# Kernel tuning notes

Hardware: AMD Instinct MI355X
Metric: run time of the kernel (lower is better)

The kernel has to match this reference:

```python
import jax, jax.numpy as jnp
import numpy as np

N_USERS = 100000
N_ITEMS = 50000
N_NODES = N_USERS + N_ITEMS
N_EDGES = 4800000
EMB_DIM = 64
N_LAYERS = 3


def setup_inputs() -> dict:
    key = jax.random.key(0)
    k1, k2, k3, k4, k5 = jax.random.split(key, 5)
    user_emb = jax.random.normal(k1, (N_USERS, EMB_DIM), dtype=jnp.float32)
    item_emb = jax.random.normal(k2, (N_ITEMS, EMB_DIM), dtype=jnp.float32)
    # COO representation of the (symmetric-normalized) adjacency matrix
    edge_src = jax.random.randint(k3, (N_EDGES,), 0, N_NODES, dtype=jnp.int32)
    edge_dst = jax.random.randint(k4, (N_EDGES,), 0, N_NODES, dtype=jnp.int32)
    edge_weight = jax.random.uniform(k5, (N_EDGES,), dtype=jnp.float32)
    return {
        "user_emb": user_emb,
        "item_emb": item_emb,
        "edge_weight": edge_weight,
        "edge_src": edge_src,
        "edge_dst": edge_dst,
    }


def _spmm(edge_src, edge_dst, edge_weight, x):
    # out[i] = sum_j A[i, j] * x[j]  with A in COO (dst=row i, src=col j)
    msgs = edge_weight[:, None] * x[edge_src]  # [E, D]
    return jax.ops.segment_sum(msgs, edge_dst, num_segments=N_NODES)


def reference(user_emb, item_emb, edge_weight, edge_src, edge_dst):
    ego = jnp.concatenate([user_emb, item_emb], axis=0)  # [N, D]
    acc = ego  # running sum over layer embeddings (layer 0 included)
    for _ in range(N_LAYERS):
        ego = _spmm(edge_src, edge_dst, edge_weight, ego)
        acc = acc + ego
    mean_emb = acc / jnp.float32(N_LAYERS + 1)  # mean over (L+1) layers
    new_user = mean_emb[:N_USERS]
    new_item = mean_emb[N_USERS:]
    return new_user, new_item
```

## Files before the change

### kernel.cpp

```cpp
#include <hip/hip_runtime.h>
#include <hip/hip_fp16.h>

#define N_USERS 100000
#define N_ITEMS 50000
#define N_NODES 150000
#define N_EDGES 4800000
#define EMB 64
#define N_LAYERS 3

#define NBKT 512
#define NPB  293
#define NREP 8
#define SUBCAP 1536
#define CAP (NREP * SUBCAP)
#define P1GRID 2344
#define INITGRID 9375

typedef unsigned int u32;
typedef unsigned short u16;
typedef u32 vu4 __attribute__((ext_vector_type(4)));
typedef u32 vu2 __attribute__((ext_vector_type(2)));
typedef float vf4 __attribute__((ext_vector_type(4)));

#define W_BITS 14
#define W_SCALE 16384.0f
#define W_INV   (1.0f / 16384.0f)
#define W_MASK  16383u

__device__ __forceinline__ float hh(u16 v) {
    return __half2float(__ushort_as_half(v));
}

struct Dec4 { u32 r0, r1, r2, r3; float w0, w1, w2, w3; };

__device__ __forceinline__ Dec4 dec_fast(vu4 p) {
    Dec4 d;
    d.r0 = p.x >> W_BITS; d.w0 = (float)(p.x & W_MASK);
    d.r1 = p.y >> W_BITS; d.w1 = (float)(p.y & W_MASK);
    d.r2 = p.z >> W_BITS; d.w2 = (float)(p.z & W_MASK);
    d.r3 = p.w >> W_BITS; d.w3 = (float)(p.w & W_MASK);
    return d;
}

__device__ __forceinline__ Dec4 dec_mask(vu4 p, int eb, int beg, int end) {
    Dec4 d;
    bool v0 = (eb + 0 >= beg) && (eb + 0 < end);
    bool v1 = (eb + 1 >= beg) && (eb + 1 < end);
    bool v2 = (eb + 2 >= beg) && (eb + 2 < end);
    bool v3 = (eb + 3 >= beg) && (eb + 3 < end);
    d.r0 = v0 ? (p.x >> W_BITS) : 0u; d.w0 = v0 ? (float)(p.x & W_MASK) : 0.f;
    d.r1 = v1 ? (p.y >> W_BITS) : 0u; d.w1 = v1 ? (float)(p.y & W_MASK) : 0.f;
    d.r2 = v2 ? (p.z >> W_BITS) : 0u; d.w2 = v2 ? (float)(p.z & W_MASK) : 0.f;
    d.r3 = v3 ? (p.w >> W_BITS) : 0u; d.w3 = v3 ? (float)(p.w & W_MASK) : 0.f;
    return d;
}

__device__ __forceinline__ Dec4 dec(vu4 p, int lo, int beg, int end, int g) {
    if (lo >= beg && lo + 16 <= end) return dec_fast(p);
    return dec_mask(p, lo + 4 * g, beg, end);
}

__device__ __forceinline__ vu4 ldp(const u32* p) {
    return __builtin_nontemporal_load((const vu4*)p);
}

__device__ __forceinline__ vu2 ldx(const char* xbase, u32 r, u32 moff) {
    return *(const vu2*)(xbase + (size_t)(r * 128u + moff));
}

__device__ __forceinline__ void fmix2(float& a0, float& a1, float w, u32 x) {
    asm("v_fma_mix_f32 %0, %1, %2, %0 op_sel:[0,0,0] op_sel_hi:[0,1,0]"
        : "+v"(a0) : "v"(w), "v"(x));
    asm("v_fma_mix_f32 %0, %1, %2, %0 op_sel:[0,1,0] op_sel_hi:[0,1,0]"
        : "+v"(a1) : "v"(w), "v"(x));
}

__device__ __forceinline__ void acc4(vu2 xv, float w,
                                     float& ax, float& ay, float& az, float& aw) {
    fmix2(ax, ay, w, xv.x);
    fmix2(az, aw, w, xv.y);
}

#define LOADX(pfx, d) \
    vu2 pfx##0 = ldx(xbase, d.r0, moff), pfx##1 = ldx(xbase, d.r1, moff), \
        pfx##2 = ldx(xbase, d.r2, moff), pfx##3 = ldx(xbase, d.r3, moff)
#define ACCX(pfx, d) \
    acc4(pfx##0, d.w0, ax, ay, az, aw); acc4(pfx##1, d.w1, ax, ay, az, aw); \
    acc4(pfx##2, d.w2, ax, ay, az, aw); acc4(pfx##3, d.w3, ax, ay, az, aw)
#define RED(v) v += __shfl_xor(v, 16); v += __shfl_xor(v, 32)

__global__ __launch_bounds__(256) void k_build1(const int4*   __restrict__ src4,
                                                const int4*   __restrict__ dst4,
                                                const float4* __restrict__ w4,
                                                int* __restrict__ cursor,
                                                u32* __restrict__ pk_arr,
                                                u16* __restrict__ ld_arr,
                                                const float4* __restrict__ user,
                                                const float4* __restrict__ item,
                                                ushort4* __restrict__ h0) {
    int tid = threadIdx.x;

    if (blockIdx.x >= P1GRID) {
        int i = (int)(blockIdx.x - P1GRID) * 256 + tid;
        const int total4 = N_NODES * EMB / 4;
        const int user4  = N_USERS * EMB / 4;
        if (i >= total4) return;
        float4 v = (i < user4) ? user[i] : item[i - user4];
        ushort4 h;
        h.x = __half_as_ushort(__float2half_rn(v.x));
        h.y = __half_as_ushort(__float2half_rn(v.y));
        h.z = __half_as_ushort(__float2half_rn(v.z));
        h.w = __half_as_ushort(__float2half_rn(v.w));
        h0[i] = h;
        return;
    }

    __shared__ int hist[NBKT];
    __shared__ int base[NBKT];
    __shared__ int bscan[NBKT];
    __shared__ int wsum[256];
    __shared__ u32 s_pk[2048];
    __shared__ u32 s_meta[2048];
    hist[tid] = 0;
    hist[tid + 256] = 0;
    __syncthreads();

    int g0 = blockIdx.x * 512 + tid * 2;
    bool act = (g0 < N_EDGES / 4);

    u32 pk[8];
    u32 meta[8];
    int rk[8];
    if (act) {
        int4 d0 = dst4[g0], d1 = dst4[g0 + 1];
        int4 s0 = src4[g0], s1 = src4[g0 + 1];
        float4 f0 = w4[g0], f1 = w4[g0 + 1];
        int   ds[8] = {d0.x, d0.y, d0.z, d0.w, d1.x, d1.y, d1.z, d1.w};
        int   ss[8] = {s0.x, s0.y, s0.z, s0.w, s1.x, s1.y, s1.z, s1.w};
        float wf[8] = {f0.x, f0.y, f0.z, f0.w, f1.x, f1.y, f1.z, f1.w};
        #pragma unroll
        for (int k = 0; k < 8; ++k) {
            u32 d  = (u32)ds[k];
            u32 b  = d / NPB;
            u32 ld = d - b * NPB;
            rk[k]  = atomicAdd(&hist[b], 1);
            u32 wq = (u32)(wf[k] * W_SCALE + 0.5f);
            if (wq > W_MASK) wq = W_MASK;
            pk[k]   = ((u32)ss[k] << W_BITS) | wq;
            meta[k] = (b << 10) | ld;
        }
    }
    __syncthreads();

    int rep = blockIdx.x & (NREP - 1);
    int hA = hist[tid];
    int hB = hist[tid + 256];
    if (hA > 0) base[tid]       = atomicAdd(&cursor[rep * NBKT + tid], hA);
    if (hB > 0) base[tid + 256] = atomicAdd(&cursor[rep * NBKT + tid + 256], hB);

    int a0 = hist[2 * tid];
    int a1 = hist[2 * tid + 1];
    wsum[tid] = a0 + a1;
    __syncthreads();
    for (int off = 1; off < 256; off <<= 1) {
        int t = 0;
        if (tid >= off) t = wsum[tid - off];
        __syncthreads();
        if (tid >= off) wsum[tid] += t;
        __syncthreads();
    }
    int exclp = wsum[tid] - (a0 + a1);
    bscan[2 * tid]     = exclp + a0;
    bscan[2 * tid + 1] = exclp + a0 + a1;
    __syncthreads();

    if (act) {
        #pragma unroll
        for (int k = 0; k < 8; ++k) {
            u32 b = meta[k] >> 10;
            int s = (bscan[b] - hist[b]) + rk[k];
            s_pk[s]   = pk[k];
            s_meta[s] = meta[k];
        }
    }
    __syncthreads();

    int total = bscan[NBKT - 1];
    #pragma unroll
    for (int k = 0; k < 8; ++k) {
        int s = k * 256 + tid;
        if (s < total) {
            u32 mt = s_meta[s];
            u32 b  = mt >> 10;
            int pos = base[b] + (s - (bscan[b] - hist[b]));
            if (pos < SUBCAP) {
                size_t slot = (size_t)b * CAP + (size_t)rep * SUBCAP + pos;
                pk_arr[slot] = s_pk[s];
                ld_arr[slot] = (u16)(mt & 1023u);
            }
        }
    }
}

extern __shared__ u32 s_pk2[];

__global__ __launch_bounds__(1024) void k_p2g(const int* __restrict__ cursor,
                                              const u32* __restrict__ pk_arr,
                                              const u16* __restrict__ ld_arr,
                                              int* __restrict__ row_ptr,
                                              u32* __restrict__ pairs,
                                              const __half* __restrict__ x,
                                              __half* __restrict__ nxt) {
    __shared__ int hist[1024];
    __shared__ int start[NPB];
    __shared__ int rbeg[NPB];
    __shared__ int rend[NPB];
    __shared__ int btot[NBKT];
    __shared__ int bsum[NBKT];
    int b = blockIdx.x;
    int tid = threadIdx.x;
    hist[tid] = 0;
    if (tid < NBKT) {
        int s = 0;
        #pragma unroll
        for (int r = 0; r < NREP; ++r) s += cursor[r * NBKT + tid];
        btot[tid] = s;
        bsum[tid] = s;
    }
    if (b == 0 && tid == 0) row_ptr[N_NODES] = N_EDGES;
    __syncthreads();
    for (int off = 1; off < NBKT; off <<= 1) {
        int t = 0;
        if (tid < NBKT && tid >= off) t = bsum[tid - off];
        __syncthreads();
        if (tid < NBKT && tid >= off) bsum[tid] += t;
        __syncthreads();
    }
    int gbase = bsum[b] - btot[b];

    int lo = b * NPB;
    int nbn = N_NODES - lo; if (nbn > NPB) nbn = NPB;

    int n[NREP];
    #pragma unroll
    for (int r = 0; r < NREP; ++r) {
        int c = cursor[r * NBKT + b];
        n[r] = (c > SUBCAP) ? SUBCAP : c;
    }

    for (int r = 0; r < NREP; ++r) {
        const u16* p = ld_arr + (size_t)b * CAP + (size_t)r * SUBCAP;
        for (int i = tid; i < n[r]; i += 1024)
            atomicAdd(&hist[p[i]], 1);
    }
    __syncthreads();

    int val = hist[tid];
    for (int off = 1; off < 1024; off <<= 1) {
        int t = 0;
        if (tid >= off) t = hist[tid - off];
        __syncthreads();
        if (tid >= off) hist[tid] += t;
        __syncthreads();
    }
    int excl = hist[tid] - val;
    if (tid < nbn) row_ptr[lo + tid] = gbase + excl;
    if (tid < NPB) {
        start[tid] = excl;
        rbeg[tid]  = excl;
        rend[tid]  = hist[tid];
    }
    __syncthreads();

    for (int r = 0; r < NREP; ++r) {
        const u16* p = ld_arr + (size_t)b * CAP + (size_t)r * SUBCAP;
        const u32* q = pk_arr + (size_t)b * CAP + (size_t)r * SUBCAP;
        for (int i = tid; i < n[r]; i += 1024) {
            int slot = atomicAdd(&start[p[i]], 1);
            s_pk2[slot] = q[i];
        }
    }
    __syncthreads();

    int total = hist[1023];
    if (tid < 16) s_pk2[total + tid] = 0;
    for (int s = tid; s < total; s += 1024)
        pairs[gbase + s] = s_pk2[s];
    __syncthreads();

    int wid  = tid >> 6;
    int lane = tid & 63;
    const int m = lane & 15;
    const int g = lane >> 4;
    const u32 moff = (u32)m << 3;
    const char* xbase = (const char*)x;

    for (int row = wid; row < nbn; row += 16) {
        int beg = rbeg[row];
        int end = rend[row];
        float ax = 0.f, ay = 0.f, az = 0.f, aw = 0.f;
        int jb = beg & ~3;
        int nb = (end - jb + 15) >> 4;
        const u32* pp = s_pk2 + jb + 4 * g;

        if (nb == 1) {
            vu4 P0 = *(const vu4*)pp;
            Dec4 d0 = dec(P0, jb, beg, end, g);
            LOADX(xa, d0);
            ACCX(xa, d0);
        } else if (nb == 2) {
            vu4 P0 = *(const vu4*)pp;
            vu4 P1 = *(const vu4*)(pp + 16);
            Dec4 d0 = dec(P0, jb, beg, end, g);
            LOADX(xa, d0);
            Dec4 d1 = dec(P1, jb + 16, beg, end, g);
            LOADX(xc, d1);
            ACCX(xa, d0);
            ACCX(xc, d1);
        } else if (nb == 3) {
            vu4 P0 = *(const vu4*)pp;
            vu4 P1 = *(const vu4*)(pp + 16);
            vu4 P2 = *(const vu4*)(pp + 32);
            Dec4 d0 = dec(P0, jb, beg, end, g);
            LOADX(xa, d0);
            Dec4 d1 = dec(P1, jb + 16, beg, end, g);
            LOADX(xc, d1);
            ACCX(xa, d0);
            Dec4 d2 = dec(P2, jb + 32, beg, end, g);
            LOADX(xd, d2);
            ACCX(xc, d1);
            ACCX(xd, d2);
        } else if (nb >= 4) {
            vu4 P0 = *(const vu4*)pp;
            vu4 P1 = *(const vu4*)(pp + 16);
            vu4 P2 = *(const vu4*)(pp + 32);
            Dec4 d0 = dec(P0, jb, beg, end, g);
            LOADX(xa, d0);
            Dec4 d1 = dec(P1, jb + 16, beg, end, g);
            LOADX(xc, d1);
            ACCX(xa, d0);
            vu4 P3 = *(const vu4*)(pp + 48);
            Dec4 d2 = dec(P2, jb + 32, beg, end, g);
            LOADX(xd, d2);
            ACCX(xc, d1);
            Dec4 d3 = dec(P3, jb + 48, beg, end, g);
            LOADX(xe, d3);
            ACCX(xd, d2);
            ACCX(xe, d3);
            for (int t = 4; t < nb; ++t) {
                vu4 Pl = *(const vu4*)(pp + (size_t)16 * t);
                Dec4 dl = dec(Pl, jb + 16 * t, beg, end, g);
                LOADX(xf, dl);
                ACCX(xf, dl);
            }
        }

        RED(ax); RED(ay); RED(az); RED(aw);

        if (lane < 16) {
            ushort4 h;
            h.x = __half_as_ushort(__float2half_rn(ax * W_INV));
            h.y = __half_as_ushort(__float2half_rn(ay * W_INV));
            h.z = __half_as_ushort(__float2half_rn(az * W_INV));
            h.w = __half_as_ushort(__float2half_rn(aw * W_INV));
            ((ushort4*)nxt)[(size_t)(lo + row) * 16 + m] = h;
        }
    }
}

template<int FIN>
__global__ __launch_bounds__(256) void k_gather(const int* __restrict__ row_ptr,
                                                const u32* __restrict__ pairs,
                                                const __half* __restrict__ x,
                                                __half* __restrict__ nxt,
                                                const ushort4* __restrict__ e0,
                                                const ushort4* __restrict__ e1,
                                                const ushort4* __restrict__ e2,
                                                float* __restrict__ outp) {
    int wave = (blockIdx.x * blockDim.x + threadIdx.x) >> 6;
    int lane = threadIdx.x & 63;
    if (wave >= N_NODES) return;

    const int m = lane & 15;
    ushort4 ega = {}, ea = {}, eb = {};
    if (FIN && lane < 16) {
        size_t idx = (size_t)wave * 16 + m;
        ega = e0[idx]; ea = e1[idx]; eb = e2[idx];
    }

    int beg = row_ptr[wave];
    int end = row_ptr[wave + 1];

    const int g = lane >> 4;
    const u32 moff = (u32)m << 3;
    const char* xbase = (const char*)x;

    float ax = 0.f, ay = 0.f, az = 0.f, aw = 0.f;

    int jb = beg & ~3;
    int nb = (end - jb + 15) >> 4;
    const u32* pp = pairs + jb + 4 * g;

    if (nb == 1) {
        vu4 P0 = ldp(pp);
        Dec4 d0 = dec(P0, jb, beg, end, g);
        LOADX(xa, d0);
        ACCX(xa, d0);
    } else if (nb == 2) {
        vu4 P0 = ldp(pp);
        vu4 P1 = ldp(pp + 16);
        Dec4 d0 = dec(P0, jb, beg, end, g);
        LOADX(xa, d0);
        Dec4 d1 = dec(P1, jb + 16, beg, end, g);
        LOADX(xc, d1);
        ACCX(xa, d0);
        ACCX(xc, d1);
    } else if (nb == 3) {
        vu4 P0 = ldp(pp);
        vu4 P1 = ldp(pp + 16);
        vu4 P2 = ldp(pp + 32);
        Dec4 d0 = dec(P0, jb, beg, end, g);
        LOADX(xa, d0);
        Dec4 d1 = dec(P1, jb + 16, beg, end, g);
        LOADX(xc, d1);
        ACCX(xa, d0);
        Dec4 d2 = dec(P2, jb + 32, beg, end, g);
        LOADX(xd, d2);
        ACCX(xc, d1);
        ACCX(xd, d2);
    } else if (nb >= 4) {
        vu4 P0 = ldp(pp);
        vu4 P1 = ldp(pp + 16);
        vu4 P2 = ldp(pp + 32);
        Dec4 d0 = dec(P0, jb, beg, end, g);
        LOADX(xa, d0);
        Dec4 d1 = dec(P1, jb + 16, beg, end, g);
        LOADX(xc, d1);
        ACCX(xa, d0);
        vu4 P3 = ldp(pp + 48);
        Dec4 d2 = dec(P2, jb + 32, beg, end, g);
        LOADX(xd, d2);
        ACCX(xc, d1);
        Dec4 d3 = dec(P3, jb + 48, beg, end, g);
        LOADX(xe, d3);
        ACCX(xd, d2);
        ACCX(xe, d3);
        for (int t = 4; t < nb; ++t) {
            vu4 Pl = ldp(pp + (size_t)16 * t);
            Dec4 dl = dec(Pl, jb + 16 * t, beg, end, g);
            LOADX(xf, dl);
            ACCX(xf, dl);
        }
    }

    RED(ax); RED(ay); RED(az); RED(aw);

    if (lane < 16) {
        if (FIN) {
            vf4 o;
            o.x = (hh(ega.x) + hh(ea.x) + hh(eb.x) + ax * W_INV) * 0.25f;
            o.y = (hh(ega.y) + hh(ea.y) + hh(eb.y) + ay * W_INV) * 0.25f;
            o.z = (hh(ega.z) + hh(ea.z) + hh(eb.z) + az * W_INV) * 0.25f;
            o.w = (hh(ega.w) + hh(ea.w) + hh(eb.w) + aw * W_INV) * 0.25f;
            __builtin_nontemporal_store(o, (vf4*)outp + (size_t)wave * 16 + m);
        } else {
            ushort4 h;
            h.x = __half_as_ushort(__float2half_rn(ax * W_INV));
            h.y = __half_as_ushort(__float2half_rn(ay * W_INV));
            h.z = __half_as_ushort(__float2half_rn(az * W_INV));
            h.w = __half_as_ushort(__float2half_rn(aw * W_INV));
            ((ushort4*)nxt)[(size_t)wave * 16 + m] = h;
        }
    }
}

__global__ void k_spmm(const int*   __restrict__ src,
                       const int*   __restrict__ dst,
                       const float* __restrict__ w,
                       const float* __restrict__ x,
                       float*       __restrict__ y) {
    long long t = (long long)blockIdx.x * blockDim.x + threadIdx.x;
    int e = (int)(t >> 4);
    if (e >= N_EDGES) return;
    int q = (int)(t & 15);
    int   s  = src[e];
    int   d  = dst[e];
    float we = w[e];
    const float4* xs = (const float4*)(x + (long long)s * EMB);
    float4 v = xs[q];
    float* yd = y + (long long)d * EMB + q * 4;
    atomicAdd(yd + 0, we * v.x);
    atomicAdd(yd + 1, we * v.y);
    atomicAdd(yd + 2, we * v.z);
    atomicAdd(yd + 3, we * v.w);
}

__global__ void k_init_f32(const float4* __restrict__ user,
                           const float4* __restrict__ item,
                           float4* __restrict__ out,
                           float4* __restrict__ cur) {
    int i = blockIdx.x * blockDim.x + threadIdx.x;
    const int total4 = N_NODES * EMB / 4;
    const int user4  = N_USERS * EMB / 4;
    if (i >= total4) return;
    float4 v = (i < user4) ? user[i] : item[i - user4];
    out[i] = v;
    cur[i] = v;
}

__global__ void k_acc(float4* __restrict__ out,
                      const float4* __restrict__ buf,
                      float scale) {
    int i = blockIdx.x * blockDim.x + threadIdx.x;
    const int total4 = N_NODES * EMB / 4;
    if (i >= total4) return;
    float4 o = out[i];
    float4 b = buf[i];
    o.x = (o.x + b.x) * scale;
    o.y = (o.y + b.y) * scale;
    o.z = (o.z + b.z) * scale;
    o.w = (o.w + b.w) * scale;
    out[i] = o;
}

extern "C" void kernel_launch(void* const* d_in, const int* in_sizes, int n_in,
                              void* d_out, int out_size, void* d_ws, size_t ws_size,
                              hipStream_t stream) {
    const float* user_emb = (const float*)d_in[0];
    const float* item_emb = (const float*)d_in[1];
    const float* edge_w   = (const float*)d_in[2];
    const int*   edge_src = (const int*)d_in[3];
    const int*   edge_dst = (const int*)d_in[4];
    float* out = (float*)d_out;

    const size_t feat_elems = (size_t)N_NODES * EMB;
    const size_t feat_bytes_f32 = feat_elems * 4;
    const size_t feat_bytes_f16 = feat_elems * 2;

    char* ws = (char*)d_ws;
    size_t off = 0;
    __half* h0 = (__half*)(ws + off); off += feat_bytes_f16;
    __half* h1 = (__half*)(ws + off); off += feat_bytes_f16;
    __half* h2 = (__half*)(ws + off); off += feat_bytes_f16;
    int* row_ptr  = (int*)(ws + off); off += ((size_t)(N_NODES + 1) * 4 + 63) / 64 * 64;
    int* cursor   = (int*)(ws + off); off += (size_t)NREP * NBKT * 4;
    u32* pk_arr = (u32*)(ws + off);   off += (size_t)NBKT * CAP * 4;
    u16* ld_arr = (u16*)(ws + off);   off += (size_t)NBKT * CAP * 2;
    u32* pairs  = (u32*)(ws + off);   off += (size_t)N_EDGES * 4 + 64;
    const size_t needed = off;

    const int block = 256;
    const int total4 = (int)(feat_elems / 4);
    const int fgrid = (total4 + block - 1) / block;
    const int bgrid = P1GRID + INITGRID;
    const int ggrid = (N_NODES + 3) / 4;

    if (ws_size >= needed) {
        (void)hipMemsetAsync(cursor, 0, (size_t)NREP * NBKT * 4, stream);

        k_build1<<<bgrid, block, 0, stream>>>((const int4*)edge_src,
                                              (const int4*)edge_dst,
                                              (const float4*)edge_w,
                                              cursor, pk_arr, ld_arr,
                                              (const float4*)user_emb,
                                              (const float4*)item_emb,
                                              (ushort4*)h0);
        k_p2g<<<NBKT, 1024, (size_t)(CAP + 16) * 4, stream>>>(cursor, pk_arr,
                                                              ld_arr, row_ptr,
                                                              pairs, h0, h1);

        k_gather<0><<<ggrid, block, 0, stream>>>(row_ptr, pairs, h1, h2,
                                                 nullptr, nullptr, nullptr,
                                                 nullptr);
        k_gather<1><<<ggrid, block, 0, stream>>>(row_ptr, pairs, h2, nullptr,
                                                 (const ushort4*)h0,
                                                 (const ushort4*)h1,
                                                 (const ushort4*)h2,
                                                 out);
    } else {
        float* buf0 = (float*)d_ws;
        float* buf1 = buf0 + feat_elems;
        k_init_f32<<<fgrid, block, 0, stream>>>((const float4*)user_emb,
                                                (const float4*)item_emb,
                                                (float4*)out, (float4*)buf0);
        float* cur = buf0;
        float* nxt = buf1;
        for (int layer = 0; layer < N_LAYERS; ++layer) {
            (void)hipMemsetAsync(nxt, 0, feat_bytes_f32, stream);
            long long threads = (long long)N_EDGES * 16;
            int grid = (int)((threads + block - 1) / block);
            k_spmm<<<grid, block, 0, stream>>>(edge_src, edge_dst, edge_w, cur, nxt);
            float scale = (layer == N_LAYERS - 1) ? (1.0f / (N_LAYERS + 1)) : 1.0f;
            k_acc<<<fgrid, block, 0, stream>>>((float4*)out, (const float4*)nxt, scale);
            float* tmp = cur; cur = nxt; nxt = tmp;
        }
    }
}
```

Baseline: 416.4 us.

## Fuse CSR build and all three gather layers into one cooperative kernel

Adds a cooperative kernel in which each of the 512 blocks builds its bucket's CSR edge list in shared memory, then runs all three propagation layers from that shared-memory copy, using grid-wide syncs between layers. This drops writing and re-reading the global row_ptr/pairs arrays and two extra kernel launches. The final layer fuses the layer mean into the output write. The cost is that occupancy is fixed at 512 resident blocks of 1024 threads, plus grid-barrier overhead. If the cooperative launch fails, it falls back to the old three-kernel path.

Result: slower. 1.001 ms (+140.5%).

```diff
diff --git a/kernel.cpp b/kernel.cpp
--- a/kernel.cpp
+++ b/kernel.cpp
@@ -1,5 +1,8 @@
 #include <hip/hip_runtime.h>
 #include <hip/hip_fp16.h>
+#include <hip/hip_cooperative_groups.h>
+
+namespace cg = cooperative_groups;
 
 #define N_USERS 100000
 #define N_ITEMS 50000
@@ -89,205 +92,18 @@
     acc4(pfx##2, d.w2, ax, ay, az, aw); acc4(pfx##3, d.w3, ax, ay, az, aw)
 #define RED(v) v += __shfl_xor(v, 16); v += __shfl_xor(v, 32)
 
-__global__ __launch_bounds__(256) void k_build1(const int4*   __restrict__ src4,
-                                                const int4*   __restrict__ dst4,
-                                                const float4* __restrict__ w4,
-                                                int* __restrict__ cursor,
-                                                u32* __restrict__ pk_arr,
-                                                u16* __restrict__ ld_arr,
-                                                const float4* __restrict__ user,
-                                                const float4* __restrict__ item,
-                                                ushort4* __restrict__ h0) {
-    int tid = threadIdx.x;
-
-    if (blockIdx.x >= P1GRID) {
-        int i = (int)(blockIdx.x - P1GRID) * 256 + tid;
-        const int total4 = N_NODES * EMB / 4;
-        const int user4  = N_USERS * EMB / 4;
-        if (i >= total4) return;
-        float4 v = (i < user4) ? user[i] : item[i - user4];
-        ushort4 h;
-        h.x = __half_as_ushort(__float2half_rn(v.x));
-        h.y = __half_as_ushort(__float2half_rn(v.y));
-        h.z = __half_as_ushort(__float2half_rn(v.z));
-        h.w = __half_as_ushort(__float2half_rn(v.w));
-        h0[i] = h;
-        return;
-    }
-
-    __shared__ int hist[NBKT];
-    __shared__ int base[NBKT];
-    __shared__ int bscan[NBKT];
-    __shared__ int wsum[256];
-    __shared__ u32 s_pk[2048];
-    __shared__ u32 s_meta[2048];
-    hist[tid] = 0;
-    hist[tid + 256] = 0;
-    __syncthreads();
-
-    int g0 = blockIdx.x * 512 + tid * 2;
-    bool act = (g0 < N_EDGES / 4);
-
-    u32 pk[8];
-    u32 meta[8];
-    int rk[8];
-    if (act) {
-        int4 d0 = dst4[g0], d1 = dst4[g0 + 1];
-        int4 s0 = src4[g0], s1 = src4[g0 + 1];
-        float4 f0 = w4[g0], f1 = w4[g0 + 1];
-        int   ds[8] = {d0.x, d0.y, d0.z, d0.w, d1.x, d1.y, d1.z, d1.w};
-        int   ss[8] = {s0.x, s0.y, s0.z, s0.w, s1.x, s1.y, s1.z, s1.w};
-        float wf[8] = {f0.x, f0.y, f0.z, f0.w, f1.x, f1.y, f1.z, f1.w};
-        #pragma unroll
-        for (int k = 0; k < 8; ++k) {
-            u32 d  = (u32)ds[k];
-            u32 b  = d / NPB;
-            u32 ld = d - b * NPB;
-            rk[k]  = atomicAdd(&hist[b], 1);
-            u32 wq = (u32)(wf[k] * W_SCALE + 0.5f);
-            if (wq > W_MASK) wq = W_MASK;
-            pk[k]   = ((u32)ss[k] << W_BITS) | wq;
-            meta[k] = (b << 10) | ld;
-        }
-    }
-    __syncthreads();
-
-    int rep = blockIdx.x & (NREP - 1);
-    int hA = hist[tid];
-    int hB = hist[tid + 256];
-    if (hA > 0) base[tid]       = atomicAdd(&cursor[rep * NBKT + tid], hA);
-    if (hB > 0) base[tid + 256] = atomicAdd(&cursor[rep * NBKT + tid + 256], hB);
-
-    int a0 = hist[2 * tid];
-    int a1 = hist[2 * tid + 1];
-    wsum[tid] = a0 + a1;
-    __syncthreads();
-    for (int off = 1; off < 256; off <<= 1) {
-        int t = 0;
-        if (tid >= off) t = wsum[tid - off];
-        __syncthreads();
-        if (tid >= off) wsum[tid] += t;
-        __syncthreads();
-    }
-    int exclp = wsum[tid] - (a0 + a1);
-    bscan[2 * tid]     = exclp + a0;
-    bscan[2 * tid + 1] = exclp + a0 + a1;
-    __syncthreads();
-
-    if (act) {
-        #pragma unroll
-        for (int k = 0; k < 8; ++k) {
-            u32 b = meta[k] >> 10;
-            int s = (bscan[b] - hist[b]) + rk[k];
-            s_pk[s]   = pk[k];
-            s_meta[s] = meta[k];
-        }
-    }
-    __syncthreads();
-
-    int total = bscan[NBKT - 1];
-    #pragma unroll
-    for (int k = 0; k < 8; ++k) {
-        int s = k * 256 + tid;
-        if (s < total) {
-            u32 mt = s_meta[s];
-            u32 b  = mt >> 10;
-            int pos = base[b] + (s - (bscan[b] - hist[b]));
-            if (pos < SUBCAP) {
-                size_t slot = (size_t)b * CAP + (size_t)rep * SUBCAP + pos;
-                pk_arr[slot] = s_pk[s];
-                ld_arr[slot] = (u16)(mt & 1023u);
-            }
-        }
-    }
-}
-
-extern __shared__ u32 s_pk2[];
-
-__global__ __launch_bounds__(1024) void k_p2g(const int* __restrict__ cursor,
-                                              const u32* __restrict__ pk_arr,
-                                              const u16* __restrict__ ld_arr,
-                                              int* __restrict__ row_ptr,
-                                              u32* __restrict__ pairs,
+template<int FIN>
+__device__ __forceinline__ void gather_bucket(const u32* __restrict__ spk,
+                                              const int* __restrict__ rbeg,
+                                              const int* __restrict__ rend,
+                                              int lo, int nbn,
                                               const __half* __restrict__ x,
-                                              __half* __restrict__ nxt) {
-    __shared__ int hist[1024];
-    __shared__ int start[NPB];
-    __shared__ int rbeg[NPB];
-    __shared__ int rend[NPB];
-    __shared__ int btot[NBKT];
-    __shared__ int bsum[NBKT];
-    int b = blockIdx.x;
-    int tid = threadIdx.x;
-    hist[tid] = 0;
-    if (tid < NBKT) {
-        int s = 0;
-        #pragma unroll
-        for (int r = 0; r < NREP; ++r) s += cursor[r * NBKT + tid];
-        btot[tid] = s;
-        bsum[tid] = s;
-    }
-    if (b == 0 && tid == 0) row_ptr[N_NODES] = N_EDGES;
-    __syncthreads();
-    for (int off = 1; off < NBKT; off <<= 1) {
-        int t = 0;
-        if (tid < NBKT && tid >= off) t = bsum[tid - off];
-        __syncthreads();
-        if (tid < NBKT && tid >= off) bsum[tid] += t;
-        __syncthreads();
-    }
-    int gbase = bsum[b] - btot[b];
-
-    int lo = b * NPB;
-    int nbn = N_NODES - lo; if (nbn > NPB) nbn = NPB;
-
-    int n[NREP];
-    #pragma unroll
-    for (int r = 0; r < NREP; ++r) {
-        int c = cursor[r * NBKT + b];
-        n[r] = (c > SUBCAP) ? SUBCAP : c;
-    }
-
-    for (int r = 0; r < NREP; ++r) {
-        const u16* p = ld_arr + (size_t)b * CAP + (size_t)r * SUBCAP;
-        for (int i = tid; i < n[r]; i += 1024)
-            atomicAdd(&hist[p[i]], 1);
-    }
-    __syncthreads();
-
-    int val = hist[tid];
-    for (int off = 1; off < 1024; off <<= 1) {
-        int t = 0;
-        if (tid >= off) t = hist[tid - off];
-        __syncthreads();
-        if (tid >= off) hist[tid] += t;
-        __syncthreads();
-    }
-    int excl = hist[tid] - val;
-    if (tid < nbn) row_ptr[lo + tid] = gbase + excl;
-    if (tid < NPB) {
-        start[tid] = excl;
-        rbeg[tid]  = excl;
-        rend[tid]  = hist[tid];
-    }
-    __syncthreads();
-
-    for (int r = 0; r < NREP; ++r) {
-        const u16* p = ld_arr + (size_t)b * CAP + (size_t)r * SUBCAP;
-        const u32* q = pk_arr + (size_t)b * CAP + (size_t)r * SUBCAP;
-        for (int i = tid; i < n[r]; i += 1024) {
-            int slot = atomicAdd(&start[p[i]], 1);
-            s_pk2[slot] = q[i];
-        }
-    }
-    __syncthreads();
-
-    int total = hist[1023];
-    if (tid < 16) s_pk2[total + tid] = 0;
-    for (int s = tid; s < total; s += 1024)
-        pairs[gbase + s] = s_pk2[s];
-    __syncthreads();
-
+                                              __half* __restrict__ nxt,
+                                              const ushort4* __restrict__ e0,
+                                              const ushort4* __restrict__ e1,
+                                              const ushort4* __restrict__ e2,
+                                              float* __restrict__ outp) {
+    int tid  = threadIdx.x;
     int wid  = tid >> 6;
     int lane = tid & 63;
     const int m = lane & 15;
@@ -296,12 +112,17 @@
     const char* xbase = (const char*)x;
 
     for (int row = wid; row < nbn; row += 16) {
+        ushort4 ega = {}, ea = {}, eb = {};
+        if (FIN && lane < 16) {
+            size_t idx = (size_t)(lo + row) * 16 + m;
+            ega = e0[idx]; ea = e1[idx]; eb = e2[idx];
+        }
         int beg = rbeg[row];
         int end = rend[row];
         float ax = 0.f, ay = 0.f, az = 0.f, aw = 0.f;
         int jb = beg & ~3;
         int nb = (end - jb + 15) >> 4;
-        const u32* pp = s_pk2 + jb + 4 * g;
+        const u32* pp = spk + jb + 4 * g;
 
         if (nb == 1) {
             vu4 P0 = *(const vu4*)pp;
@@ -358,14 +179,306 @@
         RED(ax); RED(ay); RED(az); RED(aw);
 
         if (lane < 16) {
-            ushort4 h;
-            h.x = __half_as_ushort(__float2half_rn(ax * W_INV));
-            h.y = __half_as_ushort(__float2half_rn(ay * W_INV));
-            h.z = __half_as_ushort(__float2half_rn(az * W_INV));
-            h.w = __half_as_ushort(__float2half_rn(aw * W_INV));
-            ((ushort4*)nxt)[(size_t)(lo + row) * 16 + m] = h;
-        }
-    }
+            if (FIN) {
+                vf4 o;
+                o.x = (hh(ega.x) + hh(ea.x) + hh(eb.x) + ax * W_INV) * 0.25f;
+                o.y = (hh(ega.y) + hh(ea.y) + hh(eb.y) + ay * W_INV) * 0.25f;
+                o.z = (hh(ega.z) + hh(ea.z) + hh(eb.z) + az * W_INV) * 0.25f;
+                o.w = (hh(ega.w) + hh(ea.w) + hh(eb.w) + aw * W_INV) * 0.25f;
+                __builtin_nontemporal_store(o, (vf4*)outp + (size_t)(lo + row) * 16 + m);
+            } else {
+                ushort4 h;
+                h.x = __half_as_ushort(__float2half_rn(ax * W_INV));
+                h.y = __half_as_ushort(__float2half_rn(ay * W_INV));
+                h.z = __half_as_ushort(__float2half_rn(az * W_INV));
+                h.w = __half_as_ushort(__float2half_rn(aw * W_INV));
+                ((ushort4*)nxt)[(size_t)(lo + row) * 16 + m] = h;
+            }
+        }
+    }
+}
+
+__global__ __launch_bounds__(256) void k_build1(const int4*   __restrict__ src4,
+                                                const int4*   __restrict__ dst4,
+                                                const float4* __restrict__ w4,
+                                                int* __restrict__ cursor,
+                                                u32* __restrict__ pk_arr,
+                                                u16* __restrict__ ld_arr,
+                                                const float4* __restrict__ user,
+                                                const float4* __restrict__ item,
+                                                ushort4* __restrict__ h0) {
+    int tid = threadIdx.x;
+
+    if (blockIdx.x >= P1GRID) {
+        int i = (int)(blockIdx.x - P1GRID) * 256 + tid;
+        const int total4 = N_NODES * EMB / 4;
+        const int user4  = N_USERS * EMB / 4;
+        if (i >= total4) return;
+        float4 v = (i < user4) ? user[i] : item[i - user4];
+        ushort4 h;
+        h.x = __half_as_ushort(__float2half_rn(v.x));
+        h.y = __half_as_ushort(__float2half_rn(v.y));
+        h.z = __half_as_ushort(__float2half_rn(v.z));
+        h.w = __half_as_ushort(__float2half_rn(v.w));
+        h0[i] = h;
+        return;
+    }
+
+    __shared__ int hist[NBKT];
+    __shared__ int base[NBKT];
+    __shared__ int bscan[NBKT];
+    __shared__ int wsum[256];
+    __shared__ u32 s_pk[2048];
+    __shared__ u32 s_meta[2048];
+    hist[tid] = 0;
+    hist[tid + 256] = 0;
+    __syncthreads();
+
+    int g0 = blockIdx.x * 512 + tid * 2;
+    bool act = (g0 < N_EDGES / 4);
+
+    u32 pk[8];
+    u32 meta[8];
+    int rk[8];
+    if (act) {
+        int4 d0 = dst4[g0], d1 = dst4[g0 + 1];
+        int4 s0 = src4[g0], s1 = src4[g0 + 1];
+        float4 f0 = w4[g0], f1 = w4[g0 + 1];
+        int   ds[8] = {d0.x, d0.y, d0.z, d0.w, d1.x, d1.y, d1.z, d1.w};
+        int   ss[8] = {s0.x, s0.y, s0.z, s0.w, s1.x, s1.y, s1.z, s1.w};
+        float wf[8] = {f0.x, f0.y, f0.z, f0.w, f1.x, f1.y, f1.z, f1.w};
+        #pragma unroll
+        for (int k = 0; k < 8; ++k) {
+            u32 d  = (u32)ds[k];
+            u32 b  = d / NPB;
+            u32 ld = d - b * NPB;
+            rk[k]  = atomicAdd(&hist[b], 1);
+            u32 wq = (u32)(wf[k] * W_SCALE + 0.5f);
+            if (wq > W_MASK) wq = W_MASK;
+            pk[k]   = ((u32)ss[k] << W_BITS) | wq;
+            meta[k] = (b << 10) | ld;
+        }
+    }
+    __syncthreads();
+
+    int rep = blockIdx.x & (NREP - 1);
+    int hA = hist[tid];
+    int hB = hist[tid + 256];
+    if (hA > 0) base[tid]       = atomicAdd(&cursor[rep * NBKT + tid], hA);
+    if (hB > 0) base[tid + 256] = atomicAdd(&cursor[rep * NBKT + tid + 256], hB);
+
+    int a0 = hist[2 * tid];
+    int a1 = hist[2 * tid + 1];
+    wsum[tid] = a0 + a1;
+    __syncthreads();
+    for (int off = 1; off < 256; off <<= 1) {
+        int t = 0;
+        if (tid >= off) t = wsum[tid - off];
+        __syncthreads();
+        if (tid >= off) wsum[tid] += t;
+        __syncthreads();
+    }
+    int exclp = wsum[tid] - (a0 + a1);
+    bscan[2 * tid]     = exclp + a0;
+    bscan[2 * tid + 1] = exclp + a0 + a1;
+    __syncthreads();
+
+    if (act) {
+        #pragma unroll
+        for (int k = 0; k < 8; ++k) {
+            u32 b = meta[k] >> 10;
+            int s = (bscan[b] - hist[b]) + rk[k];
+            s_pk[s]   = pk[k];
+            s_meta[s] = meta[k];
+        }
+    }
+    __syncthreads();
+
+    int total = bscan[NBKT - 1];
+    #pragma unroll
+    for (int k = 0; k < 8; ++k) {
+        int s = k * 256 + tid;
+        if (s < total) {
+            u32 mt = s_meta[s];
+            u32 b  = mt >> 10;
+            int pos = base[b] + (s - (bscan[b] - hist[b]));
+            if (pos < SUBCAP) {
+                size_t slot = (size_t)b * CAP + (size_t)rep * SUBCAP + pos;
+                pk_arr[slot] = s_pk[s];
+                ld_arr[slot] = (u16)(mt & 1023u);
+            }
+        }
+    }
+}
+
+extern __shared__ u32 s_pk2[];
+
+__global__ __launch_bounds__(1024, 8)
+void k_fused(const int* __restrict__ cursor,
+             const u32* __restrict__ pk_arr,
+             const u16* __restrict__ ld_arr,
+             const __half* __restrict__ h0,
+             __half* __restrict__ h1,
+             __half* __restrict__ h2,
+             float* __restrict__ outp) {
+    __shared__ int hist[1024];
+    __shared__ int start[NPB];
+    __shared__ int rbeg[NPB];
+    __shared__ int rend[NPB];
+    int b = blockIdx.x;
+    int tid = threadIdx.x;
+    hist[tid] = 0;
+
+    int lo = b * NPB;
+    int nbn = N_NODES - lo; if (nbn > NPB) nbn = NPB;
+
+    int n[NREP];
+    #pragma unroll
+    for (int r = 0; r < NREP; ++r) {
+        int c = cursor[r * NBKT + b];
+        n[r] = (c > SUBCAP) ? SUBCAP : c;
+    }
+    __syncthreads();
+
+    for (int r = 0; r < NREP; ++r) {
+        const u16* p = ld_arr + (size_t)b * CAP + (size_t)r * SUBCAP;
+        for (int i = tid; i < n[r]; i += 1024)
+            atomicAdd(&hist[p[i]], 1);
+    }
+    __syncthreads();
+
+    int val = hist[tid];
+    for (int off = 1; off < 1024; off <<= 1) {
+        int t = 0;
+        if (tid >= off) t = hist[tid - off];
+        __syncthreads();
+        if (tid >= off) hist[tid] += t;
+        __syncthreads();
+    }
+    int excl = hist[tid] - val;
+    if (tid < NPB) {
+        start[tid] = excl;
+        rbeg[tid]  = excl;
+        rend[tid]  = hist[tid];
+    }
+    __syncthreads();
+
+    for (int r = 0; r < NREP; ++r) {
+        const u16* p = ld_arr + (size_t)b * CAP + (size_t)r * SUBCAP;
+        const u32* q = pk_arr + (size_t)b * CAP + (size_t)r * SUBCAP;
+        for (int i = tid; i < n[r]; i += 1024) {
+            int slot = atomicAdd(&start[p[i]], 1);
+            s_pk2[slot] = q[i];
+        }
+    }
+    __syncthreads();
+    int total = hist[1023];
+    if (tid < 16) s_pk2[total + tid] = 0;
+    __syncthreads();
+
+    cg::grid_group grid = cg::this_grid();
+
+    gather_bucket<0>(s_pk2, rbeg, rend, lo, nbn, h0, h1,
+                     nullptr, nullptr, nullptr, nullptr);
+    __threadfence();
+    grid.sync();
+
+    gather_bucket<0>(s_pk2, rbeg, rend, lo, nbn, h1, h2,
+                     nullptr, nullptr, nullptr, nullptr);
+    __threadfence();
+    grid.sync();
+
+    gather_bucket<1>(s_pk2, rbeg, rend, lo, nbn, h2, nullptr,
+                     (const ushort4*)h0, (const ushort4*)h1,
+                     (const ushort4*)h2, outp);
+}
+
+__global__ __launch_bounds__(1024) void k_p2g(const int* __restrict__ cursor,
+                                              const u32* __restrict__ pk_arr,
+                                              const u16* __restrict__ ld_arr,
+                                              int* __restrict__ row_ptr,
+                                              u32* __restrict__ pairs,
+                                              const __half* __restrict__ x,
+                                              __half* __restrict__ nxt) {
+    __shared__ int hist[1024];
+    __shared__ int start[NPB];
+    __shared__ int rbeg[NPB];
+    __shared__ int rend[NPB];
+    __shared__ int btot[NBKT];
+    __shared__ int bsum[NBKT];
+    int b = blockIdx.x;
+    int tid = threadIdx.x;
+    hist[tid] = 0;
+    if (tid < NBKT) {
+        int s = 0;
+        #pragma unroll
+        for (int r = 0; r < NREP; ++r) s += cursor[r * NBKT + tid];
+        btot[tid] = s;
+        bsum[tid] = s;
+    }
+    if (b == 0 && tid == 0) row_ptr[N_NODES] = N_EDGES;
+    __syncthreads();
+    for (int off = 1; off < NBKT; off <<= 1) {
+        int t = 0;
+        if (tid < NBKT && tid >= off) t = bsum[tid - off];
+        __syncthreads();
+        if (tid < NBKT && tid >= off) bsum[tid] += t;
+        __syncthreads();
+    }
+    int gbase = bsum[b] - btot[b];
+
+    int lo = b * NPB;
+    int nbn = N_NODES - lo; if (nbn > NPB) nbn = NPB;
+
+    int n[NREP];
+    #pragma unroll
+    for (int r = 0; r < NREP; ++r) {
+        int c = cursor[r * NBKT + b];
+        n[r] = (c > SUBCAP) ? SUBCAP : c;
+    }
+
+    for (int r = 0; r < NREP; ++r) {
+        const u16* p = ld_arr + (size_t)b * CAP + (size_t)r * SUBCAP;
+        for (int i = tid; i < n[r]; i += 1024)
+            atomicAdd(&hist[p[i]], 1);
+    }
+    __syncthreads();
+
+    int val = hist[tid];
+    for (int off = 1; off < 1024; off <<= 1) {
+        int t = 0;
+        if (tid >= off) t = hist[tid - off];
+        __syncthreads();
+        if (tid >= off) hist[tid] += t;
+        __syncthreads();
+    }
+    int excl = hist[tid] - val;
+    if (tid < nbn) row_ptr[lo + tid] = gbase + excl;
+    if (tid < NPB) {
+        start[tid] = excl;
+        rbeg[tid]  = excl;
+        rend[tid]  = hist[tid];
+    }
+    __syncthreads();
+
+    for (int r = 0; r < NREP; ++r) {
+        const u16* p = ld_arr + (size_t)b * CAP + (size_t)r * SUBCAP;
+        const u32* q = pk_arr + (size_t)b * CAP + (size_t)r * SUBCAP;
+        for (int i = tid; i < n[r]; i += 1024) {
+            int slot = atomicAdd(&start[p[i]], 1);
+            s_pk2[slot] = q[i];
+        }
+    }
+    __syncthreads();
+
+    int total = hist[1023];
+    if (tid < 16) s_pk2[total + tid] = 0;
+    for (int s = tid; s < total; s += 1024)
+        pairs[gbase + s] = s_pk2[s];
+    __syncthreads();
+
+    gather_bucket<0>(s_pk2, rbeg, rend, lo, nbn, x, nxt,
+                     nullptr, nullptr, nullptr, nullptr);
 }
 
 template<int FIN>
@@ -565,18 +678,35 @@
                                               (const float4*)user_emb,
                                               (const float4*)item_emb,
                                               (ushort4*)h0);
-        k_p2g<<<NBKT, 1024, (size_t)(CAP + 16) * 4, stream>>>(cursor, pk_arr,
-                                                              ld_arr, row_ptr,
-                                                              pairs, h0, h1);
-
-        k_gather<0><<<ggrid, block, 0, stream>>>(row_ptr, pairs, h1, h2,
-                                                 nullptr, nullptr, nullptr,
-                                                 nullptr);
-        k_gather<1><<<ggrid, block, 0, stream>>>(row_ptr, pairs, h2, nullptr,
-                                                 (const ushort4*)h0,
-                                                 (const ushort4*)h1,
-                                                 (const ushort4*)h2,
-                                                 out);
+
+        const int*  a_cursor = cursor;
+        const u32*  a_pk     = pk_arr;
+        const u16*  a_ld     = ld_arr;
+        const __half* a_h0   = h0;
+        __half*     a_h1     = h1;
+        __half*     a_h2     = h2;
+        float*      a_out    = out;
+        void* kargs[] = {(void*)&a_cursor, (void*)&a_pk, (void*)&a_ld,
+                         (void*)&a_h0, (void*)&a_h1, (void*)&a_h2,
+                         (void*)&a_out};
+        hipError_t ce = hipLaunchCooperativeKernel(
+            reinterpret_cast<const void*>(&k_fused),
+            dim3(NBKT), dim3(1024), kargs,
+            (unsigned)((CAP + 16) * 4), stream);
+
+        if (ce != hipSuccess) {
+            (void)hipGetLastError();
+            k_p2g<<<NBKT, 1024, (size_t)(CAP + 16) * 4, stream>>>(
+                cursor, pk_arr, ld_arr, row_ptr, pairs, h0, h1);
+            k_gather<0><<<ggrid, block, 0, stream>>>(row_ptr, pairs, h1, h2,
+                                                     nullptr, nullptr, nullptr,
+                                                     nullptr);
+            k_gather<1><<<ggrid, block, 0, stream>>>(row_ptr, pairs, h2, nullptr,
+                                                     (const ushort4*)h0,
+                                                     (const ushort4*)h1,
+                                                     (const ushort4*)h2,
+                                                     out);
+        }
     } else {
         float* buf0 = (float*)d_ws;
         float* buf1 = buf0 + feat_elems;
```
